# Kernel tuning notes

Hardware: AMD Instinct MI355X
Metric: run time of the kernel (lower is better)

Reference implementation:

```python
import jax, jax.numpy as jnp
import numpy as np

N = 20000       # num_nodes
E = 200000      # ~ N*N*0.0005 directed edges from erdos_renyi
IN = 64         # in_channels
HID = 128       # hidden_channels (per head)
H = 4           # heads
OUT = 10        # out_channels
K1 = 10000      # ceil(0.5*N) nodes kept by pool1 (single graph -> static)
K2 = 5000       # ceil(0.5*K1) kept by pool2
NEG_SLOPE = 0.2 # PyG GATConv default negative_slope


def setup_inputs() -> dict:
    key = jax.random.key(0)
    ks = jax.random.split(key, 16)
    def glorot(k, shp, fan):
        return (jax.random.normal(k, shp, jnp.float32) / np.sqrt(fan)).astype(jnp.float32)
    x = jax.random.normal(ks[0], (N, IN), jnp.float32)
    edge_index = jax.random.randint(ks[1], (2, E), 0, N, dtype=jnp.int32)
    batch = jnp.zeros((N,), jnp.int32)
    W1 = glorot(ks[2], (IN, H * HID), IN)
    a_src1 = glorot(ks[3], (H, HID), HID)
    a_dst1 = glorot(ks[4], (H, HID), HID)
    b1 = jnp.zeros((H * HID,), jnp.float32)
    pw1 = glorot(ks[5], (H * HID,), H * HID)
    W2 = glorot(ks[6], (H * HID, H * HID), H * HID)
    a_src2 = glorot(ks[7], (H, HID), HID)
    a_dst2 = glorot(ks[8], (H, HID), HID)
    b2 = jnp.zeros((H * HID,), jnp.float32)
    pw2 = glorot(ks[9], (H * HID,), H * HID)
    Wl = glorot(ks[10], (H * HID, OUT), H * HID)
    bl = jnp.zeros((OUT,), jnp.float32)
    return dict(x=x, edge_index=edge_index, batch=batch,
                W1=W1, a_src1=a_src1, a_dst1=a_dst1, b1=b1, pw1=pw1,
                W2=W2, a_src2=a_src2, a_dst2=a_dst2, b2=b2, pw2=pw2,
                Wl=Wl, bl=bl)


def _gat(x, src, dst, emask, W, a_src, a_dst, bias):
    """PyG GATConv: gather -> LeakyReLU edge score -> scatter-softmax over dst -> scatter-add.
    Self-loops added (PyG default). emask marks valid edges (invalid edges point at node 0)."""
    n = x.shape[0]
    Hh, C = a_src.shape
    h = (x @ W).reshape(n, Hh, C)                      # [n,H,C]
    asrc = jnp.einsum('nhc,hc->nh', h, a_src)          # [n,H]
    adst = jnp.einsum('nhc,hc->nh', h, a_dst)
    loops = jnp.arange(n, dtype=src.dtype)
    sa = jnp.concatenate([src, loops])                 # [E+n]
    da = jnp.concatenate([dst, loops])
    ma = jnp.concatenate([emask, jnp.ones((n,), bool)])
    logit = jax.nn.leaky_relu(asrc[sa] + adst[da], negative_slope=NEG_SLOPE)  # [E+n,H]
    logit = jnp.where(ma[:, None], logit, -1e9)
    mx = jax.ops.segment_max(logit, da, num_segments=n)        # every node has a self-loop
    e = jnp.where(ma[:, None], jnp.exp(logit - mx[da]), 0.0)
    den = jax.ops.segment_sum(e, da, num_segments=n)
    alpha = e / den[da]                                         # [E+n,H]
    msg = (alpha[:, :, None] * h[sa]).reshape(-1, Hh * C)       # [E+n,H*C]
    return jax.ops.segment_sum(msg, da, num_segments=n) + bias  # concat heads + bias


def _topk_pool(x, src, dst, emask, w, k):
    """PyG TopKPooling (single graph): score = tanh(x.w/||w||), keep top-k nodes,
    scale kept features by score, relabel & mask edges between kept nodes."""
    score = jnp.tanh((x @ w) / jnp.linalg.norm(w))     # [n]
    vals, perm = jax.lax.top_k(score, k)
    xn = x[perm] * vals[:, None]                       # [k,F]
    remap = jnp.full((x.shape[0],), -1, jnp.int32).at[perm].set(jnp.arange(k, dtype=jnp.int32))
    s2 = remap[src]
    d2 = remap[dst]
    m2 = emask & (s2 >= 0) & (d2 >= 0)
    return xn, jnp.where(m2, s2, 0), jnp.where(m2, d2, 0), m2


def reference(x, edge_index, batch, W1, a_src1, a_dst1, b1, pw1,
              W2, a_src2, a_dst2, b2, pw2, Wl, bl):
    src = edge_index[0]
    dst = edge_index[1]
    mask = jnp.ones((src.shape[0],), bool)
    h = jax.nn.elu(_gat(x, src, dst, mask, W1, a_src1, a_dst1, b1))
    h, src, dst, mask = _topk_pool(h, src, dst, mask, pw1, K1)
    h = jax.nn.elu(_gat(h, src, dst, mask, W2, a_src2, a_dst2, b2))
    h, src, dst, mask = _topk_pool(h, src, dst, mask, pw2, K2)
    g = jnp.mean(h, axis=0, keepdims=True)             # global_mean_pool, single graph
    return g @ Wl + bl                                  # [1, OUT]
```

## Files before the change

kernel.cpp:

```cpp
#include <hip/hip_runtime.h>
#include <math.h>

#define N_NODES 20000
#define E_EDGES 200000
#define K1_KEEP 10000
#define K2_KEEP 5000
#define HIDC 128
#define NHEAD 4
#define FDIM 512
#define NEG 0.2f
#define BSTRIDE 64
#define SELCAP 20
#define MPAD 10112
#define MPAD1 20096
#define FR_GRID 250
#define FR_RPB 40

typedef _Float16 half8 __attribute__((ext_vector_type(8)));
typedef _Float16 half4 __attribute__((ext_vector_type(4)));
typedef float f32x4 __attribute__((ext_vector_type(4)));

__device__ __forceinline__ float leaky(float x){ return x > 0.f ? x : NEG * x; }
__device__ __forceinline__ float elu(float x){ return x > 0.f ? x : expm1f(x); }
__device__ __forceinline__ unsigned ordkey(float f){
    unsigned u = __float_as_uint(f);
    return (u & 0x80000000u) ? ~u : (u | 0x80000000u);
}

__global__ __launch_bounds__(256) void prep_all(const float* __restrict__ x,
        _Float16* __restrict__ X0, _Float16* __restrict__ X1,
        const float* __restrict__ W1, _Float16* __restrict__ B10, _Float16* __restrict__ B11,
        const float* __restrict__ W2, _Float16* __restrict__ B20, _Float16* __restrict__ B21,
        int* __restrict__ ctmp, int cn,
        const float* __restrict__ cw, float* __restrict__ cinvn)
{
    int bid = blockIdx.x;
    int t = threadIdx.x;
    if (bid < 628){
        int tid = bid * 256 + t;
        int r = tid >> 3, c8 = (tid & 7) << 3;
        half8 v0 = (half8)0, v1 = (half8)0;
        if (r < N_NODES){
            const float4* p = reinterpret_cast<const float4*>(&x[(size_t)r * 64 + c8]);
            float4 x0 = p[0], x1 = p[1];
            float vals[8] = {x0.x, x0.y, x0.z, x0.w, x1.x, x1.y, x1.z, x1.w};
#pragma unroll
            for (int j = 0; j < 8; ++j){
                _Float16 h = (_Float16)vals[j];
                v0[j] = h;
                v1[j] = (_Float16)(vals[j] - (float)h);
            }
        }
        if (r < MPAD1){
            *reinterpret_cast<half8*>(&X0[(size_t)r * 64 + c8]) = v0;
            *reinterpret_cast<half8*>(&X1[(size_t)r * 64 + c8]) = v1;
        }
    } else if (bid < 660){
        __shared__ float tile[32][33];
        int b = bid - 628;
        int bn = b & 15, bk = b >> 4;
        int n0 = bn * 32, k0 = bk * 32;
        int j = t & 31, i0 = t >> 5;
#pragma unroll
        for (int ii = 0; ii < 32; ii += 8)
            tile[i0 + ii][j] = W1[(size_t)(k0 + i0 + ii) * 512 + n0 + j];
        __syncthreads();
#pragma unroll
        for (int ii = 0; ii < 32; ii += 8){
            float v = tile[j][i0 + ii];
            _Float16 h0 = (_Float16)v;
            _Float16 h1 = (_Float16)(v - (float)h0);
            size_t o = (size_t)(n0 + i0 + ii) * 64 + k0 + j;
            B10[o] = h0; B11[o] = h1;
        }
    } else if (bid < 739){
        int i = (bid - 660) * 256 + t;
        if (i < cn) ctmp[i] = 0;
    } else if (bid == 739){
        __shared__ float redc[4];
        float s = cw[t] * cw[t] + cw[t + 256] * cw[t + 256];
#pragma unroll
        for (int off = 32; off > 0; off >>= 1) s += __shfl_xor(s, off);
        if ((t & 63) == 0) redc[t >> 6] = s;
        __syncthreads();
        if (t == 0) *cinvn = rsqrtf(redc[0] + redc[1] + redc[2] + redc[3]);
    } else {
        __shared__ float tile[32][33];
        int b = bid - 740;
        int bn = b & 15, bk = b >> 4;
        int n0 = bn * 32, k0 = bk * 32;
        int j = t & 31, i0 = t >> 5;
#pragma unroll
        for (int ii = 0; ii < 32; ii += 8)
            tile[i0 + ii][j] = W2[(size_t)(k0 + i0 + ii) * 512 + n0 + j];
        __syncthreads();
#pragma unroll
        for (int ii = 0; ii < 32; ii += 8){
            float v = tile[j][i0 + ii];
            _Float16 h0 = (_Float16)v;
            _Float16 h1 = (_Float16)(v - (float)h0);
            size_t o = (size_t)(n0 + i0 + ii) * 512 + k0 + j;
            B20[o] = h0; B21[o] = h1;
        }
    }
}

__global__ __launch_bounds__(256) void prep_a2(const float* __restrict__ out1,
        const int* __restrict__ remap, const float* __restrict__ score,
        _Float16* __restrict__ A0, _Float16* __restrict__ A1)
{
    int tid = blockIdx.x * 256 + threadIdx.x;
    int o = tid >> 6, kq = (tid & 63) << 3;
    if (o < N_NODES){
        int r = remap[o];
        if (r < 0) return;
        float sc = score[o];
        const float4* p = reinterpret_cast<const float4*>(&out1[(size_t)o * 512 + kq]);
        float4 x0 = p[0], x1 = p[1];
        float vals[8] = {x0.x, x0.y, x0.z, x0.w, x1.x, x1.y, x1.z, x1.w};
        half8 v0, v1;
#pragma unroll
        for (int j = 0; j < 8; ++j){
            float v = vals[j] * sc;
            _Float16 h = (_Float16)v;
            v0[j] = h;
            v1[j] = (_Float16)(v - (float)h);
        }
        *reinterpret_cast<half8*>(&A0[(size_t)r * 512 + kq]) = v0;
        *reinterpret_cast<half8*>(&A1[(size_t)r * 512 + kq]) = v1;
    } else {
        int r = K1_KEEP + (o - N_NODES);
        if (r < MPAD){
            *reinterpret_cast<half8*>(&A0[(size_t)r * 512 + kq]) = (half8)0;
            *reinterpret_cast<half8*>(&A1[(size_t)r * 512 + kq]) = (half8)0;
        }
    }
}

template<int KK>
__global__ __launch_bounds__(256, 2) void gemm_mfma(
        const _Float16* __restrict__ A0, const _Float16* __restrict__ A1,
        const _Float16* __restrict__ B0, const _Float16* __restrict__ B1,
        const float* __restrict__ avS, const float* __restrict__ avD,
        _Float16* __restrict__ C, float* __restrict__ asrc, float* __restrict__ adst,
        int nrows)
{
    __shared__ _Float16 smem[2][4][128][32];
    int t = threadIdx.x;
    int l = t & 63, w = t >> 6;
    int wr = w >> 1, wc = w & 1;
    int bidn = blockIdx.x & 3, bidm = blockIdx.x >> 2;
    int row0 = bidm * 128, col0 = bidn * 128;

    const _Float16* plane = (w == 0) ? A0 : (w == 1) ? A1 : (w == 2) ? B0 : B1;
    int prow0 = (w < 2) ? row0 : col0;
    int mloc = l >> 2;
    int gsw = (l & 3) ^ (mloc & 3);
    const _Float16* gbase = plane + (size_t)(prow0 + mloc) * KK + gsw * 8;

    f32x4 acc[4][4];
#pragma unroll
    for (int m = 0; m < 4; ++m)
#pragma unroll
        for (int n = 0; n < 4; ++n) acc[m][n] = (f32x4){0.f, 0.f, 0.f, 0.f};

    auto stage = [&](int buf, int chunk){
        const _Float16* src = gbase + chunk * 32;
        char* db = (char*)&smem[buf][w][0][0];
#pragma unroll
        for (int i = 0; i < 8; ++i)
            __builtin_amdgcn_global_load_lds(
                (const __attribute__((address_space(1))) void*)(src + (size_t)i * (KK * 16)),
                (__attribute__((address_space(3))) void*)(db + i * 1024), 16, 0, 0);
    };

    int rb = (l & 15) * 64 + (((l >> 4) ^ (l & 3)) * 16);
    const char* sb = (const char*)smem;

    constexpr int NCH = KK / 32;
    stage(0, 0);
    __syncthreads();
    for (int c = 0; c < NCH; ++c){
        int buf = c & 1;
        if (c < NCH - 1) stage(buf ^ 1, c + 1);
        const char* base = sb + buf * 32768;
        half8 a0[4], a1[4], b0[4], b1[4];
#pragma unroll
        for (int m = 0; m < 4; ++m){
            a0[m] = *(const half8*)(base +         wr * 4096 + m * 1024 + rb);
            a1[m] = *(const half8*)(base +  8192 + wr * 4096 + m * 1024 + rb);
            b0[m] = *(const half8*)(base + 16384 + wc * 4096 + m * 1024 + rb);
            b1[m] = *(const half8*)(base + 24576 + wc * 4096 + m * 1024 + rb);
        }
#pragma unroll
        for (int m = 0; m < 4; ++m)
#pragma unroll
            for (int n = 0; n < 4; ++n)
                acc[m][n] = __builtin_amdgcn_mfma_f32_16x16x32_f16(a0[m], b0[n], acc[m][n], 0, 0, 0);
#pragma unroll
        for (int m = 0; m < 4; ++m)
#pragma unroll
            for (int n = 0; n < 4; ++n)
                acc[m][n] = __builtin_amdgcn_mfma_f32_16x16x32_f16(a0[m], b1[n], acc[m][n], 0, 0, 0);
#pragma unroll
        for (int m = 0; m < 4; ++m)
#pragma unroll
            for (int n = 0; n < 4; ++n)
                acc[m][n] = __builtin_amdgcn_mfma_f32_16x16x32_f16(a1[m], b0[n], acc[m][n], 0, 0, 0);
        __syncthreads();
    }

    int head = bidn;
    const float* asv = avS + head * HIDC + wc * 64;
    const float* adv = avD + head * HIDC + wc * 64;
    int lc = l & 15, lg = l >> 4;
    int rbase = row0 + wr * 64;
    int cbase = col0 + wc * 64;
#pragma unroll
    for (int m = 0; m < 4; ++m){
#pragma unroll
        for (int q = 0; q < 4; ++q){
            int row = rbase + m * 16 + lg * 4 + q;
            bool ok = row < nrows;
            float s = 0.f, d = 0.f;
#pragma unroll
            for (int n = 0; n < 4; ++n){
                float v = acc[m][n][q];
                int cc = n * 16 + lc;
                if (ok) C[(size_t)row * 512 + cbase + cc] = (_Float16)v;
                s += v * asv[cc];
                d += v * adv[cc];
            }
#pragma unroll
            for (int off = 1; off < 16; off <<= 1){
                s += __shfl_xor(s, off);
                d += __shfl_xor(d, off);
            }
            if (ok && lc == 0){
                asrc[row * 8 + head * 2 + wc] = s;
                adst[row * 8 + head * 2 + wc] = d;
            }
        }
    }
}

__global__ void edge_fill(const int* __restrict__ src, const int* __restrict__ dst, int e,
                          int* __restrict__ tmp, int* __restrict__ csr){
    int i = blockIdx.x * 256 + threadIdx.x;
    if (i >= e) return;
    int d = dst[i];
    int pos = atomicAdd(&tmp[d], 1);
    if (pos < BSTRIDE) csr[d * BSTRIDE + pos] = src[i];
}

template<bool FILTER>
__global__ __launch_bounds__(256) void gat_fused(const _Float16* __restrict__ h,
        const float* __restrict__ asrc, const float* __restrict__ adst,
        const int* __restrict__ degs, const int* __restrict__ csr,
        const int* __restrict__ remap,
        const float* __restrict__ bias, const float* __restrict__ pw,
        const float* __restrict__ invn, float* __restrict__ out,
        float* __restrict__ score, int n)
{
    int o = blockIdx.x * 4 + (threadIdx.x >> 6);
    int lane = threadIdx.x & 63;
    if (o >= n) return;
    int node, od;
    if (FILTER){
        node = remap[o];
        if (node < 0) return;
        od = o;
    } else {
        node = o; od = o;
    }
    int deg = degs[od]; if (deg > BSTRIDE) deg = BSTRIDE;
    int e0 = od * BSTRIDE;
    int ph = lane & 3;
    int pe = lane >> 2;
    float adn, sown;
    {
        float2 dv = *reinterpret_cast<const float2*>(&adst[(size_t)node * 8 + ph * 2]);
        float2 sv = *reinterpret_cast<const float2*>(&asrc[(size_t)node * 8 + ph * 2]);
        adn = dv.x + dv.y; sown = sv.x + sv.y;
    }
    float slog = leaky(sown + adn);
    int sreg[4];
    float mx = slog;
#pragma unroll
    for (int blk = 0; blk < 4; ++blk){
        int j = blk * 16 + pe;
        int s = -1;
        if (j < deg){
            s = csr[e0 + j];
            if (FILTER) s = remap[s];
            if (s >= 0){
                float2 v = *reinterpret_cast<const float2*>(&asrc[(size_t)s * 8 + ph * 2]);
                mx = fmaxf(mx, leaky(v.x + v.y + adn));
            }
        }
        sreg[blk] = s;
    }
#pragma unroll
    for (int off = 4; off < 64; off <<= 1) mx = fmaxf(mx, __shfl_xor(mx, off));
    float aexp[4];
    float lsum = 0.f;
#pragma unroll
    for (int blk = 0; blk < 4; ++blk){
        float ex = 0.f;
        int s = sreg[blk];
        if (s >= 0){
            float2 v = *reinterpret_cast<const float2*>(&asrc[(size_t)s * 8 + ph * 2]);
            ex = expf(leaky(v.x + v.y + adn) - mx);
        }
        aexp[blk] = ex;
        lsum += ex;
    }
#pragma unroll
    for (int off = 4; off < 64; off <<= 1) lsum += __shfl_xor(lsum, off);
    float es  = expf(slog - mx);
    float inv = 1.f / (lsum + es);

    int f0 = lane * 8;
    int hf = lane >> 4;
    float invh  = __shfl(inv, hf);
    float aself = __shfl(es, hf) * invh;
    float4 acc0, acc1;
    {
        half8 v = *reinterpret_cast<const half8*>(&h[(size_t)node * FDIM + f0]);
        acc0 = make_float4(aself * (float)v[0], aself * (float)v[1],
                           aself * (float)v[2], aself * (float)v[3]);
        acc1 = make_float4(aself * (float)v[4], aself * (float)v[5],
                           aself * (float)v[6], aself * (float)v[7]);
    }
#pragma unroll
    for (int blk = 0; blk < 4; ++blk){
        int base = blk * 16;
        if (base >= deg) break;
        int cnt = deg - base; if (cnt > 16) cnt = 16;
        for (int e = 0; e < cnt; ++e){
            int s = __shfl(sreg[blk], e * 4);
            if (FILTER && s < 0) continue;
            float al = __shfl(aexp[blk], e * 4 + hf) * invh;
            half8 u = *reinterpret_cast<const half8*>(&h[(size_t)s * FDIM + f0]);
            acc0.x += al * (float)u[0]; acc0.y += al * (float)u[1];
            acc0.z += al * (float)u[2]; acc0.w += al * (float)u[3];
            acc1.x += al * (float)u[4]; acc1.y += al * (float)u[5];
            acc1.z += al * (float)u[6]; acc1.w += al * (float)u[7];
        }
    }
    const float4* bp = reinterpret_cast<const float4*>(&bias[f0]);
    float4 b0 = bp[0], b1 = bp[1];
    float4 o0 = make_float4(elu(acc0.x + b0.x), elu(acc0.y + b0.y),
                            elu(acc0.z + b0.z), elu(acc0.w + b0.w));
    float4 o1 = make_float4(elu(acc1.x + b1.x), elu(acc1.y + b1.y),
                            elu(acc1.z + b1.z), elu(acc1.w + b1.w));
    float4* op = reinterpret_cast<float4*>(&out[(size_t)node * FDIM + f0]);
    op[0] = o0; op[1] = o1;
    const float4* wp = reinterpret_cast<const float4*>(&pw[f0]);
    float4 w0 = wp[0], w1 = wp[1];
    float s = o0.x * w0.x + o0.y * w0.y + o0.z * w0.z + o0.w * w0.w
            + o1.x * w1.x + o1.y * w1.y + o1.z * w1.z + o1.w * w1.w;
#pragma unroll
    for (int off = 32; off > 0; off >>= 1) s += __shfl_xor(s, off);
    if (lane == 0) score[node] = tanhf(s * (*invn));
}

__global__ __launch_bounds__(1024) void select_compact(const float* __restrict__ score,
        int n, int k, int* __restrict__ remap,
        float* __restrict__ zbuf, int zn,
        const float* __restrict__ w, float* __restrict__ invn)
{
    __shared__ unsigned hist[4][4096];
    __shared__ unsigned wsum[16];
    __shared__ unsigned s_prefix, s_rem;
    __shared__ float red2[16];
    int t = threadIdx.x;
    int wv = t >> 6;
    int lane = t & 63;
    int hc = wv >> 2;
    unsigned keys[SELCAP];
#pragma unroll
    for (int j = 0; j < SELCAP; ++j){
        int i = t + j * 1024;
        keys[j] = (i < n) ? ordkey(score[i]) : 0u;
    }
    if (t == 0){ s_prefix = 0u; s_rem = (unsigned)k; }
    for (int i = t; i < 4 * 4096; i += 1024) ((unsigned*)hist)[i] = 0u;
    if (zbuf && t < zn) zbuf[t] = 0.f;
    __syncthreads();

#pragma unroll
    for (int j = 0; j < SELCAP; ++j){
        int i = t + j * 1024;
        if (i < n) atomicAdd(&hist[hc][keys[j] >> 20], 1u);
    }
    __syncthreads();
    {
        unsigned rem = s_rem;
        unsigned c[4]; unsigned sown = 0;
#pragma unroll
        for (int b = 0; b < 4; ++b){
            int bin = t * 4 + b;
            c[b] = hist[0][bin] + hist[1][bin] + hist[2][bin] + hist[3][bin];
            sown += c[b];
        }
        unsigned v = sown;
#pragma unroll
        for (int off = 1; off < 64; off <<= 1){
            unsigned o = __shfl_down(v, off);
            if (lane + off < 64) v += o;
        }
        if (lane == 0) wsum[wv] = v;
        __syncthreads();
        unsigned hi = 0;
        for (int q = wv + 1; q < 16; ++q) hi += wsum[q];
        unsigned run = v + hi - sown;
#pragma unroll
        for (int b = 3; b >= 0; --b){
            unsigned suf = run + c[b];
            if (suf >= rem && run < rem){
                s_prefix = (unsigned)(t * 4 + b) << 20;
                s_rem = rem - run;
            }
            run = suf;
        }
    }
    __syncthreads();
    unsigned prefA = s_prefix;
    for (int i = t; i < 4 * 4096; i += 1024) ((unsigned*)hist)[i] = 0u;
    __syncthreads();

#pragma unroll
    for (int j = 0; j < SELCAP; ++j){
        int i = t + j * 1024;
        if (i < n && (keys[j] >> 20) == (prefA >> 20))
            atomicAdd(&hist[hc][(keys[j] >> 8) & 0xFFFu], 1u);
    }
    __syncthreads();
    {
        unsigned rem = s_rem;
        unsigned c[4]; unsigned sown = 0;
#pragma unroll
        for (int b = 0; b < 4; ++b){
            int bin = t * 4 + b;
            c[b] = hist[0][bin] + hist[1][bin] + hist[2][bin] + hist[3][bin];
            sown += c[b];
        }
        unsigned v = sown;
#pragma unroll
        for (int off = 1; off < 64; off <<= 1){
            unsigned o = __shfl_down(v, off);
            if (lane + off < 64) v += o;
        }
        if (lane == 0) wsum[wv] = v;
        __syncthreads();
        unsigned hi = 0;
        for (int q = wv + 1; q < 16; ++q) hi += wsum[q];
        unsigned run = v + hi - sown;
#pragma unroll
        for (int b = 3; b >= 0; --b){
            unsigned suf = run + c[b];
            if (suf >= rem && run < rem){
                s_prefix = prefA | ((unsigned)(t * 4 + b) << 8);
                s_rem = rem - run;
            }
            run = suf;
        }
    }
    __syncthreads();
    unsigned prefB = s_prefix;
    for (int i = t; i < 4 * 4096; i += 1024) ((unsigned*)hist)[i] = 0u;
    __syncthreads();

#pragma unroll
    for (int j = 0; j < SELCAP; ++j){
        int i = t + j * 1024;
        if (i < n && (keys[j] >> 8) == (prefB >> 8))
            atomicAdd(&hist[hc][keys[j] & 255u], 1u);
    }
    __syncthreads();
    {
        unsigned rem = s_rem;
        unsigned cC = 0, vC = 0;
        if (t < 256){
            cC = hist[0][t] + hist[1][t] + hist[2][t] + hist[3][t];
            vC = cC;
#pragma unroll
            for (int off = 1; off < 64; off <<= 1){
                unsigned o = __shfl_down(vC, off);
                if ((t & 63) + off < 64) vC += o;
            }
            if ((t & 63) == 0) wsum[t >> 6] = vC;
        }
        __syncthreads();
        if (t < 256){
#pragma unroll
            for (int q = 0; q < 4; ++q)
                if (q > (t >> 6)) vC += wsum[q];
            unsigned nxt = vC - cC;
            if (vC >= rem && nxt < rem){
                s_prefix = prefB | (unsigned)t;
                s_rem = rem - nxt;
            }
        }
    }
    __syncthreads();

    unsigned T = s_prefix, ties = s_rem;
    int ngt = 0, ntie = 0;
#pragma unroll
    for (int j = 0; j < SELCAP; ++j){
        int i = t + j * 1024;
        if (i >= n) continue;
        if (keys[j] > T) ++ngt;
        else if (keys[j] == T) ++ntie;
    }
    unsigned pk = ((unsigned)ngt << 16) | (unsigned)ntie;
    unsigned v2 = pk;
#pragma unroll
    for (int off = 1; off < 64; off <<= 1){
        unsigned o = __shfl_up(v2, off);
        if (lane >= off) v2 += o;
    }
    if (lane == 63) wsum[wv] = v2;
    __syncthreads();
    unsigned base = 0;
    for (int q = 0; q < wv; ++q) base += wsum[q];
    unsigned excl = base + v2 - pk;
    int gpos = (int)(excl >> 16);
    int tpos = (int)(excl & 0xFFFFu);
    int gtot = k - (int)ties;
#pragma unroll
    for (int j = 0; j < SELCAP; ++j){
        int i = t + j * 1024;
        if (i >= n) continue;
        unsigned key = keys[j];
        int pos = -1;
        if (key > T) pos = gpos++;
        else if (key == T){
            int tr = tpos++;
            if (tr < (int)ties) pos = gtot + tr;
        }
        remap[i] = pos;
    }
    if (w){
        float s = (t < 512) ? w[t] * w[t] : 0.f;
#pragma unroll
        for (int off = 32; off > 0; off >>= 1) s += __shfl_xor(s, off);
        if ((t & 63) == 0) red2[wv] = s;
        __syncthreads();
        if (t == 0){
            float a = 0.f;
            for (int i = 0; i < 16; ++i) a += red2[i];
            *invn = rsqrtf(a);
        }
    }
}

__global__ __launch_bounds__(512) void final_reduce(const float* __restrict__ x,
        const int* __restrict__ remap, const float* __restrict__ score,
        float* __restrict__ acc, const float* __restrict__ Wl,
        const float* __restrict__ bl, int* __restrict__ done,
        float* __restrict__ outp)
{
    __shared__ float gsh[512];
    __shared__ int last;
    int t = threadIdx.x;
    int r0 = blockIdx.x * FR_RPB;
    float a = 0.f;
#pragma unroll
    for (int i = 0; i < FR_RPB; i += 4){
        int rr = r0 + i;
        float s0 = (remap[rr + 0] >= 0) ? score[rr + 0] : 0.f;
        float s1 = (remap[rr + 1] >= 0) ? score[rr + 1] : 0.f;
        float s2 = (remap[rr + 2] >= 0) ? score[rr + 2] : 0.f;
        float s3 = (remap[rr + 3] >= 0) ? score[rr + 3] : 0.f;
        float v0 = x[(size_t)(rr + 0) * FDIM + t];
        float v1 = x[(size_t)(rr + 1) * FDIM + t];
        float v2 = x[(size_t)(rr + 2) * FDIM + t];
        float v3 = x[(size_t)(rr + 3) * FDIM + t];
        a += v0 * s0 + v1 * s1 + v2 * s2 + v3 * s3;
    }
    gsh[t] = a;
    __syncthreads();
    int wv = t >> 6, lane = t & 63;
#pragma unroll
    for (int rep = 0; rep < 2; ++rep){
        int w = wv + rep * 8;
        if (w >= 10) break;
        float s = 0.f;
#pragma unroll
        for (int f = 0; f < 8; ++f) s += gsh[lane + f * 64] * Wl[(lane + f * 64) * 10 + w];
#pragma unroll
        for (int off = 32; off > 0; off >>= 1) s += __shfl_xor(s, off);
        if (lane == 0) atomicAdd(&acc[w * 32], s);
    }
    __syncthreads();
    if (t == 0){
        __threadfence();
        last = (atomicAdd(done, 1) == (int)gridDim.x - 1);
    }
    __syncthreads();
    if (!last) return;
    if (t < 10){
        float v = __hip_atomic_load(&acc[t * 32], __ATOMIC_RELAXED,
                                    __HIP_MEMORY_SCOPE_AGENT);
        outp[t] = v * (1.0f / K2_KEEP) + bl[t];
    }
}

extern "C" void kernel_launch(void* const* d_in, const int* in_sizes, int n_in,
                              void* d_out, int out_size, void* d_ws, size_t ws_size,
                              hipStream_t stream)
{
    (void)in_sizes; (void)n_in; (void)out_size; (void)ws_size;
    const float* x   = (const float*)d_in[0];
    const int*   ei  = (const int*)  d_in[1];
    const float* W1  = (const float*)d_in[3];
    const float* as1 = (const float*)d_in[4];
    const float* ad1 = (const float*)d_in[5];
    const float* b1  = (const float*)d_in[6];
    const float* pw1 = (const float*)d_in[7];
    const float* W2  = (const float*)d_in[8];
    const float* as2 = (const float*)d_in[9];
    const float* ad2 = (const float*)d_in[10];
    const float* b2  = (const float*)d_in[11];
    const float* pw2 = (const float*)d_in[12];
    const float* Wl  = (const float*)d_in[13];
    const float* bl  = (const float*)d_in[14];
    const int* src1 = ei;
    const int* dst1 = ei + E_EDGES;

    char* wsb = (char*)d_ws;
    size_t off = 0;
    auto alloc = [&](size_t bytes) -> char* {
        char* p = wsb + off;
        off += (bytes + 255) & ~(size_t)255;
        return p;
    };
    _Float16* h1f = (_Float16*)alloc((size_t)N_NODES * FDIM * 2);
    float* out1 = (float*)alloc((size_t)N_NODES * FDIM * 4);
    float* asrc = (float*)alloc((size_t)N_NODES * 8 * 4);
    float* adst = (float*)alloc((size_t)N_NODES * 8 * 4);
    float* score= (float*)alloc((size_t)N_NODES * 4);
    float* invn = (float*)alloc(4);
    int* tmp  = (int*)alloc((size_t)N_NODES * 4);
    int* csr  = (int*)alloc((size_t)N_NODES * BSTRIDE * 4);
    int* remap= (int*)alloc((size_t)N_NODES * 4);
    float* racc = (float*)alloc(336 * 4);
    _Float16* a0p = (_Float16*)alloc((size_t)MPAD * FDIM * 2);
    _Float16* a1p = (_Float16*)alloc((size_t)MPAD * FDIM * 2);
    _Float16* w2t0 = (_Float16*)alloc((size_t)FDIM * FDIM * 2);
    _Float16* w2t1 = (_Float16*)alloc((size_t)FDIM * FDIM * 2);
    _Float16* x0p = (_Float16*)alloc((size_t)MPAD1 * 64 * 2);
    _Float16* x1p = (_Float16*)alloc((size_t)MPAD1 * 64 * 2);
    _Float16* w1t0 = (_Float16*)alloc((size_t)FDIM * 64 * 2);
    _Float16* w1t1 = (_Float16*)alloc((size_t)FDIM * 64 * 2);
    _Float16* h2f = h1f;
    float* out2 = out1;
    int* done = (int*)(racc + 320);

    prep_all<<<996, 256, 0, stream>>>(x, x0p, x1p, W1, w1t0, w1t1,
            W2, w2t0, w2t1, tmp, N_NODES, pw1, invn);
    gemm_mfma<64><<<(MPAD1 / 128) * 4, 256, 0, stream>>>(x0p, x1p, w1t0, w1t1,
            as1, ad1, h1f, asrc, adst, N_NODES);
    edge_fill<<<(E_EDGES + 255) / 256, 256, 0, stream>>>(src1, dst1, E_EDGES, tmp, csr);
    gat_fused<false><<<(N_NODES + 3) / 4, 256, 0, stream>>>(h1f, asrc, adst, tmp, csr,
            nullptr, b1, pw1, invn, out1, score, N_NODES);

    select_compact<<<1, 1024, 0, stream>>>(score, N_NODES, K1_KEEP, remap,
                                           nullptr, 0, pw2, invn);

    {
        int nth = (N_NODES + (MPAD - K1_KEEP)) * 64;
        prep_a2<<<nth / 256, 256, 0, stream>>>(out1, remap, score, a0p, a1p);
    }
    gemm_mfma<512><<<(MPAD / 128) * 4, 256, 0, stream>>>(a0p, a1p, w2t0, w2t1,
            as2, ad2, h2f, asrc, adst, K1_KEEP);
    gat_fused<true><<<(N_NODES + 3) / 4, 256, 0, stream>>>(h2f, asrc, adst, tmp, csr,
            remap, b2, pw2, invn, out2, score, N_NODES);

    select_compact<<<1, 1024, 0, stream>>>(score, K1_KEEP, K2_KEEP, remap,
                                           racc, 336, nullptr, nullptr);
    final_reduce<<<FR_GRID, 512, 0, stream>>>(out2, remap, score, racc, Wl,
                                              bl, done, (float*)d_out);
}
```

Baseline: 264.5 us.

## Parallelize top-k radix select across blocks with global atomics and grid barriers

Replaces the single 1024-thread block radix select with a multi-block kernel where each block handles 512 scores, merges histograms into global buffers via atomics, and synchronizes using a software grid barrier. The final rank placement uses global atomic counters for per-block bases. Buffers are zeroed in an extra prep_all block range. This removes the serial single-block bottleneck but adds barrier spin costs and makes kept-node ordering depend on atomic arrival order.

```diff
diff --git a/kernel.cpp b/kernel.cpp
--- a/kernel.cpp
+++ b/kernel.cpp
@@ -10,11 +10,11 @@
 #define FDIM 512
 #define NEG 0.2f
 #define BSTRIDE 64
-#define SELCAP 20
 #define MPAD 10112
 #define MPAD1 20096
 #define FR_GRID 250
 #define FR_RPB 40
+#define SELWORDS 8512
 
 typedef _Float16 half8 __attribute__((ext_vector_type(8)));
 typedef _Float16 half4 __attribute__((ext_vector_type(4)));
@@ -32,7 +32,8 @@
         const float* __restrict__ W1, _Float16* __restrict__ B10, _Float16* __restrict__ B11,
         const float* __restrict__ W2, _Float16* __restrict__ B20, _Float16* __restrict__ B21,
         int* __restrict__ ctmp, int cn,
-        const float* __restrict__ cw, float* __restrict__ cinvn)
+        const float* __restrict__ cw, float* __restrict__ cinvn,
+        unsigned* __restrict__ selbuf)
 {
     int bid = blockIdx.x;
     int t = threadIdx.x;
@@ -84,7 +85,7 @@
         if ((t & 63) == 0) redc[t >> 6] = s;
         __syncthreads();
         if (t == 0) *cinvn = rsqrtf(redc[0] + redc[1] + redc[2] + redc[3]);
-    } else {
+    } else if (bid < 996){
         __shared__ float tile[32][33];
         int b = bid - 740;
         int bn = b & 15, bk = b >> 4;
@@ -102,6 +103,9 @@
             size_t o = (size_t)(n0 + i0 + ii) * 512 + k0 + j;
             B20[o] = h0; B21[o] = h1;
         }
+    } else {
+        int i = (bid - 996) * 256 + t;
+        if (i < 2 * SELWORDS) selbuf[i] = 0u;
     }
 }
 
@@ -365,194 +369,217 @@
     if (lane == 0) score[node] = tanhf(s * (*invn));
 }
 
-__global__ __launch_bounds__(1024) void select_compact(const float* __restrict__ score,
-        int n, int k, int* __restrict__ remap,
+__global__ __launch_bounds__(256) void select3(const float* __restrict__ score,
+        int n, int k, int nb, int* __restrict__ remap,
+        unsigned* __restrict__ bA, unsigned* __restrict__ bB, unsigned* __restrict__ bC,
+        unsigned* __restrict__ meta,
         float* __restrict__ zbuf, int zn,
         const float* __restrict__ w, float* __restrict__ invn)
 {
-    __shared__ unsigned hist[4][4096];
-    __shared__ unsigned wsum[16];
-    __shared__ unsigned s_prefix, s_rem;
-    __shared__ float red2[16];
-    int t = threadIdx.x;
-    int wv = t >> 6;
-    int lane = t & 63;
-    int hc = wv >> 2;
-    unsigned keys[SELCAP];
-#pragma unroll
-    for (int j = 0; j < SELCAP; ++j){
-        int i = t + j * 1024;
-        keys[j] = (i < n) ? ordkey(score[i]) : 0u;
-    }
-    if (t == 0){ s_prefix = 0u; s_rem = (unsigned)k; }
-    for (int i = t; i < 4 * 4096; i += 1024) ((unsigned*)hist)[i] = 0u;
-    if (zbuf && t < zn) zbuf[t] = 0.f;
-    __syncthreads();
-
-#pragma unroll
-    for (int j = 0; j < SELCAP; ++j){
-        int i = t + j * 1024;
-        if (i < n) atomicAdd(&hist[hc][keys[j] >> 20], 1u);
-    }
-    __syncthreads();
-    {
-        unsigned rem = s_rem;
-        unsigned c[4]; unsigned sown = 0;
-#pragma unroll
-        for (int b = 0; b < 4; ++b){
-            int bin = t * 4 + b;
-            c[b] = hist[0][bin] + hist[1][bin] + hist[2][bin] + hist[3][bin];
-            sown += c[b];
-        }
-        unsigned v = sown;
+    __shared__ unsigned hb[4096];
+    __shared__ unsigned wt[4];
+    __shared__ unsigned sPref, sR;
+    __shared__ unsigned gbaseS, tbaseS;
+    __shared__ float red2[4];
+    int t = threadIdx.x, lane = t & 63, wv = t >> 6;
+    int bid = blockIdx.x;
+    int i0 = bid * 512 + t, i1 = i0 + 256;
+    bool v0 = i0 < n, v1 = i1 < n;
+    unsigned key0 = v0 ? ordkey(score[i0]) : 0u;
+    unsigned key1 = v1 ? ordkey(score[i1]) : 0u;
+
+    auto gbar = [&](){
+        __syncthreads();
+        if (t == 0){
+            __threadfence();
+            unsigned g = __hip_atomic_load(&meta[56], __ATOMIC_RELAXED,
+                                           __HIP_MEMORY_SCOPE_AGENT);
+            if (__hip_atomic_fetch_add(&meta[48], 1u, __ATOMIC_ACQ_REL,
+                                       __HIP_MEMORY_SCOPE_AGENT) == (unsigned)(nb - 1)){
+                __hip_atomic_store(&meta[48], 0u, __ATOMIC_RELAXED,
+                                   __HIP_MEMORY_SCOPE_AGENT);
+                __hip_atomic_store(&meta[56], g + 1u, __ATOMIC_RELEASE,
+                                   __HIP_MEMORY_SCOPE_AGENT);
+            } else {
+                while (__hip_atomic_load(&meta[56], __ATOMIC_ACQUIRE,
+                                         __HIP_MEMORY_SCOPE_AGENT) == g)
+                    __builtin_amdgcn_s_sleep(1);
+            }
+            __threadfence();
+        }
+        __syncthreads();
+    };
+
+    for (int i = t; i < 4096; i += 256) hb[i] = 0u;
+    __syncthreads();
+    if (v0) atomicAdd(&hb[key0 >> 20], 1u);
+    if (v1) atomicAdd(&hb[key1 >> 20], 1u);
+    __syncthreads();
+    for (int i = t; i < 4096; i += 256){
+        unsigned c = hb[i];
+        if (c) atomicAdd(&bA[i], c);
+    }
+    gbar();
+    {
+        unsigned rem = (unsigned)k;
+        unsigned c[16]; unsigned csum = 0;
+#pragma unroll
+        for (int j = 0; j < 16; ++j){
+            c[j] = __hip_atomic_load(&bA[t * 16 + j], __ATOMIC_RELAXED,
+                                     __HIP_MEMORY_SCOPE_AGENT);
+            csum += c[j];
+        }
+        unsigned v = csum;
 #pragma unroll
         for (int off = 1; off < 64; off <<= 1){
             unsigned o = __shfl_down(v, off);
             if (lane + off < 64) v += o;
         }
-        if (lane == 0) wsum[wv] = v;
+        if (lane == 0) wt[wv] = v;
         __syncthreads();
         unsigned hi = 0;
-        for (int q = wv + 1; q < 16; ++q) hi += wsum[q];
-        unsigned run = v + hi - sown;
-#pragma unroll
-        for (int b = 3; b >= 0; --b){
-            unsigned suf = run + c[b];
+        for (int q = wv + 1; q < 4; ++q) hi += wt[q];
+        unsigned run = v + hi - csum;
+#pragma unroll
+        for (int j = 15; j >= 0; --j){
+            unsigned suf = run + c[j];
             if (suf >= rem && run < rem){
-                s_prefix = (unsigned)(t * 4 + b) << 20;
-                s_rem = rem - run;
+                sPref = (unsigned)(t * 16 + j) << 20;
+                sR = rem - run;
             }
             run = suf;
         }
     }
     __syncthreads();
-    unsigned prefA = s_prefix;
-    for (int i = t; i < 4 * 4096; i += 1024) ((unsigned*)hist)[i] = 0u;
-    __syncthreads();
-
-#pragma unroll
-    for (int j = 0; j < SELCAP; ++j){
-        int i = t + j * 1024;
-        if (i < n && (keys[j] >> 20) == (prefA >> 20))
-            atomicAdd(&hist[hc][(keys[j] >> 8) & 0xFFFu], 1u);
-    }
-    __syncthreads();
-    {
-        unsigned rem = s_rem;
-        unsigned c[4]; unsigned sown = 0;
-#pragma unroll
-        for (int b = 0; b < 4; ++b){
-            int bin = t * 4 + b;
-            c[b] = hist[0][bin] + hist[1][bin] + hist[2][bin] + hist[3][bin];
-            sown += c[b];
-        }
-        unsigned v = sown;
+    unsigned prefA = sPref, remA = sR;
+    __syncthreads();
+
+    for (int i = t; i < 4096; i += 256) hb[i] = 0u;
+    __syncthreads();
+    if (v0 && (key0 >> 20) == (prefA >> 20)) atomicAdd(&hb[(key0 >> 8) & 0xFFFu], 1u);
+    if (v1 && (key1 >> 20) == (prefA >> 20)) atomicAdd(&hb[(key1 >> 8) & 0xFFFu], 1u);
+    __syncthreads();
+    for (int i = t; i < 4096; i += 256){
+        unsigned c = hb[i];
+        if (c) atomicAdd(&bB[i], c);
+    }
+    gbar();
+    {
+        unsigned rem = remA;
+        unsigned c[16]; unsigned csum = 0;
+#pragma unroll
+        for (int j = 0; j < 16; ++j){
+            c[j] = __hip_atomic_load(&bB[t * 16 + j], __ATOMIC_RELAXED,
+                                     __HIP_MEMORY_SCOPE_AGENT);
+            csum += c[j];
+        }
+        unsigned v = csum;
 #pragma unroll
         for (int off = 1; off < 64; off <<= 1){
             unsigned o = __shfl_down(v, off);
             if (lane + off < 64) v += o;
         }
-        if (lane == 0) wsum[wv] = v;
+        if (lane == 0) wt[wv] = v;
         __syncthreads();
         unsigned hi = 0;
-        for (int q = wv + 1; q < 16; ++q) hi += wsum[q];
-        unsigned run = v + hi - sown;
-#pragma unroll
-        for (int b = 3; b >= 0; --b){
-            unsigned suf = run + c[b];
+        for (int q = wv + 1; q < 4; ++q) hi += wt[q];
+        unsigned run = v + hi - csum;
+#pragma unroll
+        for (int j = 15; j >= 0; --j){
+            unsigned suf = run + c[j];
             if (suf >= rem && run < rem){
-                s_prefix = prefA | ((unsigned)(t * 4 + b) << 8);
-                s_rem = rem - run;
+                sPref = prefA | ((unsigned)(t * 16 + j) << 8);
+                sR = rem - run;
             }
             run = suf;
         }
     }
     __syncthreads();
-    unsigned prefB = s_prefix;
-    for (int i = t; i < 4 * 4096; i += 1024) ((unsigned*)hist)[i] = 0u;
-    __syncthreads();
-
-#pragma unroll
-    for (int j = 0; j < SELCAP; ++j){
-        int i = t + j * 1024;
-        if (i < n && (keys[j] >> 8) == (prefB >> 8))
-            atomicAdd(&hist[hc][keys[j] & 255u], 1u);
-    }
-    __syncthreads();
-    {
-        unsigned rem = s_rem;
-        unsigned cC = 0, vC = 0;
-        if (t < 256){
-            cC = hist[0][t] + hist[1][t] + hist[2][t] + hist[3][t];
-            vC = cC;
-#pragma unroll
-            for (int off = 1; off < 64; off <<= 1){
-                unsigned o = __shfl_down(vC, off);
-                if ((t & 63) + off < 64) vC += o;
-            }
-            if ((t & 63) == 0) wsum[t >> 6] = vC;
-        }
-        __syncthreads();
-        if (t < 256){
-#pragma unroll
-            for (int q = 0; q < 4; ++q)
-                if (q > (t >> 6)) vC += wsum[q];
-            unsigned nxt = vC - cC;
-            if (vC >= rem && nxt < rem){
-                s_prefix = prefB | (unsigned)t;
-                s_rem = rem - nxt;
-            }
-        }
-    }
-    __syncthreads();
-
-    unsigned T = s_prefix, ties = s_rem;
-    int ngt = 0, ntie = 0;
-#pragma unroll
-    for (int j = 0; j < SELCAP; ++j){
-        int i = t + j * 1024;
-        if (i >= n) continue;
-        if (keys[j] > T) ++ngt;
-        else if (keys[j] == T) ++ntie;
-    }
-    unsigned pk = ((unsigned)ngt << 16) | (unsigned)ntie;
-    unsigned v2 = pk;
+    unsigned prefB = sPref, remB = sR;
+    __syncthreads();
+
+    for (int i = t; i < 256; i += 256) hb[i] = 0u;
+    __syncthreads();
+    if (v0 && (key0 >> 8) == (prefB >> 8)) atomicAdd(&hb[key0 & 255u], 1u);
+    if (v1 && (key1 >> 8) == (prefB >> 8)) atomicAdd(&hb[key1 & 255u], 1u);
+    __syncthreads();
+    {
+        unsigned c = hb[t];
+        if (c) atomicAdd(&bC[t], c);
+    }
+    gbar();
+    {
+        unsigned rem = remB;
+        unsigned cC = __hip_atomic_load(&bC[t], __ATOMIC_RELAXED,
+                                        __HIP_MEMORY_SCOPE_AGENT);
+        unsigned vC = cC;
+#pragma unroll
+        for (int off = 1; off < 64; off <<= 1){
+            unsigned o = __shfl_down(vC, off);
+            if (lane + off < 64) vC += o;
+        }
+        if (lane == 0) wt[wv] = vC;
+        __syncthreads();
+        unsigned hi = 0;
+        for (int q = wv + 1; q < 4; ++q) hi += wt[q];
+        vC += hi;
+        unsigned nxt = vC - cC;
+        if (vC >= rem && nxt < rem){
+            sPref = prefB | (unsigned)t;
+            sR = rem - nxt;
+        }
+    }
+    __syncthreads();
+    unsigned T = sPref, ties = sR;
+
+    int g0 = (v0 && key0 > T) ? 1 : 0, e0 = (v0 && key0 == T) ? 1 : 0;
+    int g1 = (v1 && key1 > T) ? 1 : 0, e1 = (v1 && key1 == T) ? 1 : 0;
+    unsigned pk = ((unsigned)(g0 + g1) << 16) | (unsigned)(e0 + e1);
+    unsigned v = pk;
 #pragma unroll
     for (int off = 1; off < 64; off <<= 1){
-        unsigned o = __shfl_up(v2, off);
-        if (lane >= off) v2 += o;
-    }
-    if (lane == 63) wsum[wv] = v2;
-    __syncthreads();
-    unsigned base = 0;
-    for (int q = 0; q < wv; ++q) base += wsum[q];
-    unsigned excl = base + v2 - pk;
-    int gpos = (int)(excl >> 16);
-    int tpos = (int)(excl & 0xFFFFu);
+        unsigned o = __shfl_up(v, off);
+        if (lane >= off) v += o;
+    }
+    if (lane == 63) wt[wv] = v;
+    __syncthreads();
+    unsigned wb = 0;
+    for (int q = 0; q < wv; ++q) wb += wt[q];
+    unsigned excl = wb + v - pk;
+    if (t == 255){
+        unsigned tot = wb + v;
+        gbaseS = atomicAdd(&meta[16], tot >> 16);
+        tbaseS = atomicAdd(&meta[32], tot & 0xFFFFu);
+    }
+    __syncthreads();
+    int gpos = (int)(gbaseS + (excl >> 16));
+    int tpos = (int)(tbaseS + (excl & 0xFFFFu));
     int gtot = k - (int)ties;
-#pragma unroll
-    for (int j = 0; j < SELCAP; ++j){
-        int i = t + j * 1024;
-        if (i >= n) continue;
-        unsigned key = keys[j];
+    if (v0){
         int pos = -1;
-        if (key > T) pos = gpos++;
-        else if (key == T){
-            int tr = tpos++;
-            if (tr < (int)ties) pos = gtot + tr;
-        }
-        remap[i] = pos;
-    }
-    if (w){
-        float s = (t < 512) ? w[t] * w[t] : 0.f;
-#pragma unroll
-        for (int off = 32; off > 0; off >>= 1) s += __shfl_xor(s, off);
-        if ((t & 63) == 0) red2[wv] = s;
-        __syncthreads();
-        if (t == 0){
-            float a = 0.f;
-            for (int i = 0; i < 16; ++i) a += red2[i];
-            *invn = rsqrtf(a);
+        if (g0) pos = gpos;
+        else if (e0 && tpos < (int)ties) pos = gtot + tpos;
+        remap[i0] = pos;
+    }
+    gpos += g0; tpos += e0;
+    if (v1){
+        int pos = -1;
+        if (g1) pos = gpos;
+        else if (e1 && tpos < (int)ties) pos = gtot + tpos;
+        remap[i1] = pos;
+    }
+    if (bid == 0){
+        if (w){
+            float s = w[t] * w[t] + w[t + 256] * w[t + 256];
+#pragma unroll
+            for (int off = 32; off > 0; off >>= 1) s += __shfl_xor(s, off);
+            if (lane == 0) red2[wv] = s;
+            __syncthreads();
+            if (t == 0) *invn = rsqrtf(red2[0] + red2[1] + red2[2] + red2[3]);
+        }
+        if (zbuf){
+            if (t < zn) zbuf[t] = 0.f;
+            if (t + 256 < zn) zbuf[t + 256] = 0.f;
         }
     }
 }
@@ -648,6 +675,7 @@
     int* csr  = (int*)alloc((size_t)N_NODES * BSTRIDE * 4);
     int* remap= (int*)alloc((size_t)N_NODES * 4);
     float* racc = (float*)alloc(336 * 4);
+    unsigned* selbuf = (unsigned*)alloc(2 * SELWORDS * 4);
     _Float16* a0p = (_Float16*)alloc((size_t)MPAD * FDIM * 2);
     _Float16* a1p = (_Float16*)alloc((size_t)MPAD * FDIM * 2);
     _Float16* w2t0 = (_Float16*)alloc((size_t)FDIM * FDIM * 2);
@@ -659,17 +687,23 @@
     _Float16* h2f = h1f;
     float* out2 = out1;
     int* done = (int*)(racc + 320);
-
-    prep_all<<<996, 256, 0, stream>>>(x, x0p, x1p, W1, w1t0, w1t1,
-            W2, w2t0, w2t1, tmp, N_NODES, pw1, invn);
+    unsigned* sb1 = selbuf;
+    unsigned* sb2 = selbuf + SELWORDS;
+
+    prep_all<<<1063, 256, 0, stream>>>(x, x0p, x1p, W1, w1t0, w1t1,
+            W2, w2t0, w2t1, tmp, N_NODES, pw1, invn, selbuf);
     gemm_mfma<64><<<(MPAD1 / 128) * 4, 256, 0, stream>>>(x0p, x1p, w1t0, w1t1,
             as1, ad1, h1f, asrc, adst, N_NODES);
     edge_fill<<<(E_EDGES + 255) / 256, 256, 0, stream>>>(src1, dst1, E_EDGES, tmp, csr);
     gat_fused<false><<<(N_NODES + 3) / 4, 256, 0, stream>>>(h1f, asrc, adst, tmp, csr,
             nullptr, b1, pw1, invn, out1, score, N_NODES);
 
-    select_compact<<<1, 1024, 0, stream>>>(score, N_NODES, K1_KEEP, remap,
-                                           nullptr, 0, pw2, invn);
+    {
+        int nb = (N_NODES + 511) / 512;
+        select3<<<nb, 256, 0, stream>>>(score, N_NODES, K1_KEEP, nb, remap,
+                sb1, sb1 + 4096, sb1 + 8192, sb1 + 8448,
+                nullptr, 0, pw2, invn);
+    }
 
     {
         int nth = (N_NODES + (MPAD - K1_KEEP)) * 64;
@@ -680,8 +714,12 @@
     gat_fused<true><<<(N_NODES + 3) / 4, 256, 0, stream>>>(h2f, asrc, adst, tmp, csr,
             remap, b2, pw2, invn, out2, score, N_NODES);
 
-    select_compact<<<1, 1024, 0, stream>>>(score, K1_KEEP, K2_KEEP, remap,
-                                           racc, 336, nullptr, nullptr);
+    {
+        int nb = (K1_KEEP + 511) / 512;
+        select3<<<nb, 256, 0, stream>>>(score, K1_KEEP, K2_KEEP, nb, remap,
+                sb2, sb2 + 4096, sb2 + 8192, sb2 + 8448,
+                racc, 336, nullptr, nullptr);
+    }
     final_reduce<<<FR_GRID, 512, 0, stream>>>(out2, remap, score, racc, Wl,
                                               bl, done, (float*)d_out);
 }
```

Result: slower. 278.8 us (+5.4%).
